# Performance work log

Measured on AMD Instinct MI355X. Metric: run time of the kernel, lower is better.

## Reference

```python
import jax, jax.numpy as jnp
import numpy as np

B, N, DEG, LOOKBACK, DIM, OUT = 256, 512, 16, 5, 64, 6
E = B * N * DEG            # 2,097,152 directed edges
NN = B * N                 # 131,072 nodes
K1 = int(np.ceil(0.8 * N))    # 410 nodes kept per graph after pool1
K2 = int(np.ceil(0.8 * K1))   # 328 nodes kept per graph after pool2


def setup_inputs():
    key = jax.random.key(0)
    ks = jax.random.split(key, 14)
    x = jax.random.normal(ks[0], (NN, LOOKBACK), jnp.float32)
    # per-graph random edges, then shift into the global node index space
    local = jax.random.randint(ks[1], (2, E), 0, N)
    offsets = jnp.repeat(jnp.arange(B, dtype=jnp.int32) * N, N * DEG)
    edge_index = local + offsets[None, :]

    def lin(k, fi, fo):
        return jax.random.normal(k, (fi, fo), jnp.float32) / np.sqrt(fi)

    return {
        "x": x,
        "edge_index": edge_index,
        "c1_Wl": lin(ks[2], LOOKBACK, DIM), "c1_bl": jnp.zeros((DIM,), jnp.float32),
        "c1_Wr": lin(ks[3], LOOKBACK, DIM),
        "pool1_w": jax.random.normal(ks[4], (DIM,), jnp.float32) / np.sqrt(DIM),
        "c2_Wl": lin(ks[5], DIM, DIM), "c2_bl": jnp.zeros((DIM,), jnp.float32),
        "c2_Wr": lin(ks[6], DIM, DIM),
        "pool2_w": jax.random.normal(ks[7], (DIM,), jnp.float32) / np.sqrt(DIM),
        "lin1_W": lin(ks[8], 2 * DIM, DIM), "lin1_b": jnp.zeros((DIM,), jnp.float32),
        "lin2_W": lin(ks[9], DIM, OUT), "lin2_b": jnp.zeros((OUT,), jnp.float32),
    }


def _sage(x, src, dst, valid, Wl, bl, Wr, n_nodes):
    # PyG SAGEConv: out = lin_l(mean_{j->i} x_j) + lin_r(x_i); empty nbhd -> 0
    msg = x[src] * valid[:, None]
    s = jax.ops.segment_sum(msg, dst, num_segments=n_nodes)
    deg = jax.ops.segment_sum(valid, dst, num_segments=n_nodes)
    mean = s / jnp.maximum(deg, 1.0)[:, None]
    return mean @ Wl + bl + x @ Wr


def _topk(x, w, nb, npg, k):
    # PyG TopKPooling: score = tanh(x.w/||w||), keep top-k per graph, scale kept rows
    score = jnp.tanh((x @ w) / jnp.linalg.norm(w))
    vals, idx = jax.lax.top_k(score.reshape(nb, npg), k)     # [nb, k]
    perm = (idx + (jnp.arange(nb) * npg)[:, None]).reshape(-1)
    return x[perm] * vals.reshape(-1, 1), perm


def _readout(x, nb, k):
    r = x.reshape(nb, k, -1)
    return jnp.concatenate([r.max(axis=1), r.mean(axis=1)], axis=1)  # [gmp | gap]


def reference(x, edge_index, c1_Wl, c1_bl, c1_Wr, pool1_w,
              c2_Wl, c2_bl, c2_Wr, pool2_w, lin1_W, lin1_b, lin2_W, lin2_b):
    src, dst = edge_index[0], edge_index[1]
    valid0 = jnp.ones((E,), jnp.float32)

    h = jax.nn.relu(_sage(x, src, dst, valid0, c1_Wl, c1_bl, c1_Wr, NN))
    h, perm1 = _topk(h, pool1_w, B, N, K1)
    x1 = _readout(h, B, K1)

    # filter_adj: remap edges to pooled node ids, mask dropped edges
    n1 = B * K1
    inv = jnp.full((NN,), -1, jnp.int32).at[perm1].set(jnp.arange(n1, dtype=jnp.int32))
    s1, d1 = inv[src], inv[dst]
    valid1 = ((s1 >= 0) & (d1 >= 0)).astype(jnp.float32)
    s1 = jnp.maximum(s1, 0)
    d1 = jnp.maximum(d1, 0)

    h = jax.nn.relu(_sage(h, s1, d1, valid1, c2_Wl, c2_bl, c2_Wr, n1))
    h, _ = _topk(h, pool2_w, B, K1, K2)
    x2 = _readout(h, B, K2)

    z = x1 + x2
    z = jax.nn.relu(z @ lin1_W + lin1_b)
    return z @ lin2_W + lin2_b
```

## Files before the change

kernel.cpp:

```cpp
#include <hip/hip_runtime.h>
#include <hip/hip_bf16.h>

#define BGR   256
#define NPG1  512
#define DEG   16
#define EPG   (NPG1 * DEG)
#define LB    5
#define DIM   64
#define OUTF  6
#define NN    (BGR * NPG1)
#define EDG   (BGR * EPG)
#define K1    410
#define K2    328
#define N1    (BGR * K1)
#define K1P   (K1 + 1)
#define NR    (BGR * K1P)
#define CSRW  48
#define CSRW1 56
#define RSTR  68
#define GRIDW (NR / 64)
#define GRIDA (N1 / 16)

__global__ __launch_bounds__(512)
void s1_csr_score_kernel(const float* __restrict__ x,
                         const int* __restrict__ eidx,
                         const float* __restrict__ Wl,
                         const float* __restrict__ bl,
                         const float* __restrict__ Wr,
                         const float* __restrict__ pw,
                         float* __restrict__ meanv,
                         float* __restrict__ sc1g) {
    __shared__ __align__(16) float xl[NPG1 * LB];
    __shared__ unsigned short lcsr[CSRW1 * NPG1];
    __shared__ int lcnt[NPG1];

    const int g = blockIdx.x, t = threadIdx.x;
    const int* __restrict__ src = eidx;
    const int* __restrict__ dst = eidx + EDG;

    {
        const float4* x4 = (const float4*)(x + (size_t)g * (NPG1 * LB));
        float4* xl4 = (float4*)xl;
        #pragma unroll
        for (int k = 0; k < 2; ++k) {
            int i = k * 512 + t;
            if (i < NPG1 * LB / 4) xl4[i] = x4[i];
        }
        lcnt[t] = 0;
    }
    __syncthreads();

    const int ebase = g * EPG;
    for (int k = 0; k < EPG / 512; ++k) {
        int e = ebase + k * 512 + t;
        int s = src[e] & (NPG1 - 1);
        int d = dst[e] & (NPG1 - 1);
        int slot = atomicAdd(&lcnt[d], 1);
        if (slot < CSRW1) lcsr[slot * NPG1 + d] = (unsigned short)s;
    }
    __syncthreads();

    const int dgf = lcnt[t];
    const int dg  = min(dgf, CSRW1);
    float s0 = 0.f, s1 = 0.f, s2 = 0.f, s3 = 0.f, s4 = 0.f;
    for (int k = 0; k < dg; ++k) {
        int s = lcsr[k * NPG1 + t];
        const float* xp = xl + s * LB;
        s0 += xp[0]; s1 += xp[1]; s2 += xp[2]; s3 += xp[3]; s4 += xp[4];
    }
    const float invd = 1.f / fmaxf((float)dgf, 1.f);
    float m[LB]  = { s0 * invd, s1 * invd, s2 * invd, s3 * invd, s4 * invd };
    float xv[LB];
    const int n = g * NPG1 + t;
    #pragma unroll
    for (int j = 0; j < LB; ++j) { xv[j] = xl[t * LB + j]; meanv[(size_t)n * LB + j] = m[j]; }

    const float4* Wl4 = (const float4*)Wl;
    const float4* Wr4 = (const float4*)Wr;
    const float4* bl4 = (const float4*)bl;
    const float4* pw4 = (const float4*)pw;
    float p = 0.f, q = 0.f;
    #pragma unroll 4
    for (int d4 = 0; d4 < DIM / 4; ++d4) {
        float4 bb = bl4[d4];
        float4 ww = pw4[d4];
        float4 h = bb;
        #pragma unroll
        for (int j = 0; j < LB; ++j) {
            float4 a = Wl4[j * (DIM / 4) + d4];
            float4 b = Wr4[j * (DIM / 4) + d4];
            h.x += m[j] * a.x + xv[j] * b.x;
            h.y += m[j] * a.y + xv[j] * b.y;
            h.z += m[j] * a.z + xv[j] * b.z;
            h.w += m[j] * a.w + xv[j] * b.w;
        }
        h.x = fmaxf(h.x, 0.f); h.y = fmaxf(h.y, 0.f);
        h.z = fmaxf(h.z, 0.f); h.w = fmaxf(h.w, 0.f);
        p += h.x * ww.x + h.y * ww.y + h.z * ww.z + h.w * ww.w;
        q += ww.x * ww.x + ww.y * ww.y + ww.z * ww.z + ww.w * ww.w;
    }
    sc1g[n] = tanhf(p / sqrtf(q));
}

__global__ __launch_bounds__(512)
void s1_rankpool_kernel(const float* __restrict__ x,
                        const float* __restrict__ meanv,
                        const float* __restrict__ sc1g,
                        const float* __restrict__ Wl,
                        const float* __restrict__ bl,
                        const float* __restrict__ Wr,
                        float* __restrict__ h1p,
                        int* __restrict__ invr,
                        float* __restrict__ x1buf) {
    __shared__ __align__(16) float sc[NPG1];
    __shared__ int   rnk[NPG1];
    __shared__ float redmx[8 * DIM];
    __shared__ float redsm[8 * DIM];

    const int g = blockIdx.x, t = threadIdx.x;
    const int wid = t >> 6, lane = t & 63;

    sc[t] = sc1g[g * NPG1 + t];
    if (t < DIM) h1p[((size_t)g * K1P + K1) * DIM + t] = 0.f;
    __syncthreads();

    {
        float my = sc[t];
        int r = 0;
        const float4* sc4 = (const float4*)sc;
        #pragma unroll 4
        for (int j4 = 0; j4 < NPG1 / 4; ++j4) {
            float4 v = sc4[j4];
            int j = 4 * j4;
            r += (v.x > my) | ((v.x == my) & (j     < t));
            r += (v.y > my) | ((v.y == my) & (j + 1 < t));
            r += (v.z > my) | ((v.z == my) & (j + 2 < t));
            r += (v.w > my) | ((v.w == my) & (j + 3 < t));
        }
        rnk[t] = r;
        invr[g * NPG1 + t] = (r < K1) ? r : -1;
    }
    __syncthreads();

    float wlv[LB], wrv[LB];
    #pragma unroll
    for (int j = 0; j < LB; ++j) { wlv[j] = Wl[j * DIM + lane]; wrv[j] = Wr[j * DIM + lane]; }
    const float blv = bl[lane];

    float mx = -INFINITY, sm = 0.f;
    for (int n = wid; n < NPG1; n += 8) {
        int r = rnk[n];
        if (r >= K1) continue;
        const float* mp = meanv + (size_t)(g * NPG1 + n) * LB;
        const float* xp = x + (size_t)(g * NPG1 + n) * LB;
        float al = 0.f, ar = 0.f;
        #pragma unroll
        for (int j = 0; j < LB; ++j) {
            al += mp[j] * wlv[j];
            ar += xp[j] * wrv[j];
        }
        float acc = fmaxf(blv + al + ar, 0.f);
        float v = acc * sc[n];
        h1p[((size_t)g * K1P + r) * DIM + lane] = v;
        mx = fmaxf(mx, v);
        sm += v;
    }
    redmx[wid * DIM + lane] = mx;
    redsm[wid * DIM + lane] = sm;
    __syncthreads();
    if (wid == 0) {
        float m2 = redmx[lane], s2 = redsm[lane];
        #pragma unroll
        for (int w = 1; w < 8; ++w) {
            m2 = fmaxf(m2, redmx[w * DIM + lane]);
            s2 += redsm[w * DIM + lane];
        }
        x1buf[g * 2 * DIM + lane]       = m2;
        x1buf[g * 2 * DIM + DIM + lane] = s2 * (1.0f / (float)K1);
    }
}

__global__ __launch_bounds__(512)
void csr2_build_kernel(const int* __restrict__ eidx,
                       const int* __restrict__ invr,
                       unsigned short* __restrict__ csr2,
                       int* __restrict__ indeg) {
    __shared__ short linv[NPG1];
    __shared__ __align__(16) unsigned short lcsr[K1 * CSRW];
    __shared__ int lcnt[K1];

    const int g = blockIdx.x, t = threadIdx.x;
    const int* __restrict__ src = eidx;
    const int* __restrict__ dst = eidx + EDG;

    if (t < NPG1) linv[t] = (short)invr[g * NPG1 + t];
    if (t < K1) lcnt[t] = 0;
    {
        const int fill = (K1 << 16) | K1;
        int* li = (int*)lcsr;
        for (int i = t; i < K1 * CSRW / 2; i += 512) li[i] = fill;
    }
    __syncthreads();

    const int ebase = g * EPG;
    for (int k = 0; k < EPG / 512; ++k) {
        int e = ebase + k * 512 + t;
        int rs = linv[src[e] & (NPG1 - 1)];
        int rd = linv[dst[e] & (NPG1 - 1)];
        if ((rs | rd) >= 0) {
            int slot = atomicAdd(&lcnt[rd], 1);
            if (slot < CSRW) lcsr[rd * CSRW + slot] = (unsigned short)rs;
        }
    }
    __syncthreads();

    {
        const int4* ls4 = (const int4*)lcsr;
        int4* gs4 = (int4*)(csr2 + (size_t)g * K1 * CSRW);
        for (int i = t; i < K1 * CSRW / 8; i += 512) gs4[i] = ls4[i];
        if (t < K1) indeg[g * K1 + t] = min(lcnt[t], CSRW);
    }
}

__global__ __launch_bounds__(256)
void gemm2_kernel(float* __restrict__ hY,
                  float* __restrict__ Yr,
                  const float* __restrict__ Wl,
                  const float* __restrict__ bl,
                  const float* __restrict__ Wr) {
    __shared__ __align__(16) float rt[64 * RSTR];

    const int t = threadIdx.x;
    const int nb = (int)blockIdx.x * 64;

    {
        const float4* G = (const float4*)&hY[(size_t)nb * DIM];
        #pragma unroll
        for (int k = 0; k < 4; ++k) {
            int c = k * 256 + t;
            int r = c >> 4, j4 = c & 15;
            *(float4*)&rt[r * RSTR + 4 * j4] = G[c];
        }
    }
    __syncthreads();

    const int lane = t & 63;
    const int wid  = __builtin_amdgcn_readfirstlane(t >> 6);
    const int cb   = (wid & 1) << 5;
    const bool isR = (wid & 2) != 0;
    const float* __restrict__ wmat = isR ? Wr : Wl;
    float* __restrict__ outp = isR ? Yr : hY;

    float rv[DIM];
    #pragma unroll
    for (int k = 0; k < DIM / 4; ++k) {
        float4 v = *(const float4*)&rt[lane * RSTR + 4 * k];
        rv[4 * k] = v.x; rv[4 * k + 1] = v.y; rv[4 * k + 2] = v.z; rv[4 * k + 3] = v.w;
    }

    float acc[32];
    #pragma unroll
    for (int c = 0; c < 32; ++c) acc[c] = 0.f;

    #pragma unroll
    for (int j = 0; j < DIM; ++j) {
        const float* __restrict__ wr_ = wmat + j * DIM + cb;
        #pragma unroll
        for (int c = 0; c < 32; ++c)
            acc[c] += rv[j] * wr_[c];
    }

    if (isR) {
        #pragma unroll
        for (int c = 0; c < 32; ++c) acc[c] += bl[cb + c];
    }

    float* orow = outp + (size_t)(nb + lane) * DIM + cb;
    #pragma unroll
    for (int k = 0; k < 8; ++k) {
        float4 v;
        v.x = acc[4 * k]; v.y = acc[4 * k + 1];
        v.z = acc[4 * k + 2]; v.w = acc[4 * k + 3];
        *(float4*)&orow[4 * k] = v;
    }
}

__global__ __launch_bounds__(256)
void gather2_kernel(const float* __restrict__ Yl,
                    float* __restrict__ Yh,
                    const unsigned short* __restrict__ csr2,
                    const int* __restrict__ indeg,
                    const float* __restrict__ pw,
                    float* __restrict__ sc2g) {
    const int t = threadIdx.x, wid = t >> 6, lane = t & 63;
    const int cid = ((int)blockIdx.x & 7) * (GRIDA / 8) + ((int)blockIdx.x >> 3);
    const int nb = __builtin_amdgcn_readfirstlane(cid * 16 + wid * 4);

    const float pwv = pw[lane];
    float q = pwv * pwv;
    #pragma unroll
    for (int o = 32; o; o >>= 1) q += __shfl_xor(q, o);
    const float inv_nrm = 1.f / sqrtf(q);

    #pragma unroll
    for (int i = 0; i < 4; ++i) {
        const int n  = nb + i;
        const int dg = indeg[n];
        const int g  = n / K1;
        const int lr = n - g * K1;
        const float* __restrict__ bp = Yl + (size_t)g * K1P * DIM;
        const int4* cr = (const int4*)(csr2 + (size_t)n * CSRW);
        float a0 = 0.f, a1 = 0.f;
        const int it = (dg + 7) >> 3;
        for (int kc = 0; kc < it; ++kc) {
            int4 wv = cr[kc];
            a0 += bp[((wv.x & 0xffff) << 6) + lane];
            a1 += bp[((wv.x >> 16)    << 6) + lane];
            a0 += bp[((wv.y & 0xffff) << 6) + lane];
            a1 += bp[((wv.y >> 16)    << 6) + lane];
            a0 += bp[((wv.z & 0xffff) << 6) + lane];
            a1 += bp[((wv.z >> 16)    << 6) + lane];
            a0 += bp[((wv.w & 0xffff) << 6) + lane];
            a1 += bp[((wv.w >> 16)    << 6) + lane];
        }
        const float invd = 1.f / fmaxf((float)dg, 1.f);
        float* yrow = Yh + (size_t)(g * K1P + lr) * DIM;
        const float h = fmaxf((a0 + a1) * invd + yrow[lane], 0.f);
        yrow[lane] = h;
        float p = h * pwv;
        #pragma unroll
        for (int o = 32; o; o >>= 1) p += __shfl_xor(p, o);
        if (lane == 0) sc2g[n] = tanhf(p * inv_nrm);
    }
}

__global__ __launch_bounds__(512)
void pool2_mlp_kernel(const float* __restrict__ sc2g,
                      const float* __restrict__ h2,
                      const float* __restrict__ x1buf,
                      const float* __restrict__ W1,
                      const float* __restrict__ b1,
                      const float* __restrict__ W2,
                      const float* __restrict__ b2,
                      float* __restrict__ out) {
    __shared__ __align__(16) float sc2[412];
    __shared__ int   rnk2[K1];
    __shared__ float redmx[8 * DIM];
    __shared__ float redsm[8 * DIM];
    __shared__ float zy[2 * DIM + DIM];

    const int g = blockIdx.x, t = threadIdx.x;
    const int wid = t >> 6, lane = t & 63;

    if (t < K1) sc2[t] = sc2g[g * K1 + t];
    if (t >= K1 && t < 412) sc2[t] = -INFINITY;
    __syncthreads();

    if (t < K1) {
        float my = sc2[t];
        int r = 0;
        const float4* sc4 = (const float4*)sc2;
        #pragma unroll 4
        for (int j4 = 0; j4 < 103; ++j4) {
            float4 v = sc4[j4];
            int j = 4 * j4;
            r += (v.x > my) | ((v.x == my) & (j     < t));
            r += (v.y > my) | ((v.y == my) & (j + 1 < t));
            r += (v.z > my) | ((v.z == my) & (j + 2 < t));
            r += (v.w > my) | ((v.w == my) & (j + 3 < t));
        }
        rnk2[t] = r;
    }
    __syncthreads();

    float mx = -INFINITY, sm = 0.f;
    for (int n = wid; n < K1; n += 8) {
        if (rnk2[n] < K2) {
            float v = h2[((size_t)g * K1P + n) * DIM + lane] * sc2[n];
            mx = fmaxf(mx, v);
            sm += v;
        }
    }
    redmx[wid * DIM + lane] = mx;
    redsm[wid * DIM + lane] = sm;
    __syncthreads();
    if (wid == 0) {
        float m2 = redmx[lane], s2 = redsm[lane];
        #pragma unroll
        for (int w = 1; w < 8; ++w) {
            m2 = fmaxf(m2, redmx[w * DIM + lane]);
            s2 += redsm[w * DIM + lane];
        }
        zy[lane]       = x1buf[g * 2 * DIM + lane]       + m2;
        zy[DIM + lane] = x1buf[g * 2 * DIM + DIM + lane] + s2 * (1.0f / (float)K2);
    }
    __syncthreads();

    if (t < DIM) {
        float a = b1[t];
        #pragma unroll 8
        for (int j = 0; j < 2 * DIM; ++j) a += zy[j] * W1[j * DIM + t];
        zy[2 * DIM + t] = fmaxf(a, 0.f);
    }
    __syncthreads();
    if (t < OUTF) {
        float a = b2[t];
        #pragma unroll
        for (int j = 0; j < DIM; ++j) a += zy[2 * DIM + j] * W2[j * OUTF + t];
        out[g * OUTF + t] = a;
    }
}

extern "C" void kernel_launch(void* const* d_in, const int* in_sizes, int n_in,
                              void* d_out, int out_size, void* d_ws, size_t ws_size,
                              hipStream_t stream) {
    (void)in_sizes; (void)n_in; (void)out_size; (void)ws_size;
    const float* x       = (const float*)d_in[0];
    const int*   eidx    = (const int*)d_in[1];
    const float* c1_Wl   = (const float*)d_in[2];
    const float* c1_bl   = (const float*)d_in[3];
    const float* c1_Wr   = (const float*)d_in[4];
    const float* pool1_w = (const float*)d_in[5];
    const float* c2_Wl   = (const float*)d_in[6];
    const float* c2_bl   = (const float*)d_in[7];
    const float* c2_Wr   = (const float*)d_in[8];
    const float* pool2_w = (const float*)d_in[9];
    const float* lin1_W  = (const float*)d_in[10];
    const float* lin1_b  = (const float*)d_in[11];
    const float* lin2_W  = (const float*)d_in[12];
    const float* lin2_b  = (const float*)d_in[13];
    float* out = (float*)d_out;

    char* w = (char*)d_ws;
    size_t off = 0;
    auto alloc = [&](size_t bytes) {
        void* p = w + off;
        off = (off + bytes + 255) & ~(size_t)255;
        return p;
    };
    float* h1p   = (float*)alloc((size_t)NR * DIM * 4);
    int*   invr  = (int*)  alloc((size_t)NN * 4);
    float* x1buf = (float*)alloc((size_t)BGR * 2 * DIM * 4);
    float* sc2g  = (float*)alloc((size_t)N1 * 4);
    int*   indeg = (int*)  alloc((size_t)N1 * 4);
    float* Yh    = (float*)alloc((size_t)NR * DIM * 4);
    char*  csreg = (char*) alloc((size_t)N1 * CSRW * 2);

    float* Yl    = h1p;
    unsigned short* csr2 = (unsigned short*)csreg;
    float* meanv = (float*)csreg;
    float* sc1g  = meanv + (size_t)NN * LB;

    s1_csr_score_kernel<<<BGR, 512, 0, stream>>>(x, eidx, c1_Wl, c1_bl, c1_Wr,
                                                 pool1_w, meanv, sc1g);
    s1_rankpool_kernel<<<BGR, 512, 0, stream>>>(x, meanv, sc1g, c1_Wl, c1_bl,
                                                c1_Wr, h1p, invr, x1buf);
    csr2_build_kernel<<<BGR, 512, 0, stream>>>(eidx, invr, csr2, indeg);
    gemm2_kernel<<<GRIDW, 256, 0, stream>>>(h1p, Yh, c2_Wl, c2_bl, c2_Wr);
    gather2_kernel<<<GRIDA, 256, 0, stream>>>(Yl, Yh, csr2, indeg, pool2_w, sc2g);
    pool2_mlp_kernel<<<BGR, 512, 0, stream>>>(sc2g, Yh, x1buf, lin1_W, lin1_b,
                                              lin2_W, lin2_b, out);
}
```

Measured before the change: 188.5 us.

## Register-tile layer-2 GEMM with transposed weights staged in LDS

A small prologue kernel transposes and concatenates the conv2 Wl and Wr matrices into one weight buffer. gemm2 now processes 128 rows per block and stages both the activation tile and the swizzled transposed weights in LDS. Each thread computes an 8x8 output micro-tile from float4 LDS reads, replacing per-lane row registers fed by uniform global weight loads. This aims to raise arithmetic intensity per LDS access and halve the block count. The costs are an extra kernel launch, more LDS per block, and float4 accesses at a 65-float row stride that are not 16-byte aligned.

New measurement: 184.3 us. -2.3%, faster.

```diff
diff --git a/kernel.cpp b/kernel.cpp
--- a/kernel.cpp
+++ b/kernel.cpp
@@ -17,8 +17,8 @@
 #define NR    (BGR * K1P)
 #define CSRW  48
 #define CSRW1 56
-#define RSTR  68
-#define GRIDW (NR / 64)
+#define RSTR  65
+#define GRIDW (NR / 128)
 #define GRIDA (N1 / 16)
 
 __global__ __launch_bounds__(512)
@@ -223,65 +223,87 @@
 }
 
 __global__ __launch_bounds__(256)
+void wtrans_kernel(const float* __restrict__ Wl,
+                   const float* __restrict__ Wr,
+                   float* __restrict__ WT) {
+    int i = blockIdx.x * 256 + threadIdx.x;
+    int c = i >> 6, j = i & 63;
+    WT[i] = (c < DIM) ? Wl[j * DIM + c] : Wr[j * DIM + (c - DIM)];
+}
+
+__global__ __launch_bounds__(256, 2)
 void gemm2_kernel(float* __restrict__ hY,
                   float* __restrict__ Yr,
-                  const float* __restrict__ Wl,
-                  const float* __restrict__ bl,
-                  const float* __restrict__ Wr) {
-    __shared__ __align__(16) float rt[64 * RSTR];
+                  const float* __restrict__ WT,
+                  const float* __restrict__ bl) {
+    __shared__ __align__(16) float rt[128 * RSTR];
+    __shared__ __align__(16) float wt[128 * DIM];
 
     const int t = threadIdx.x;
-    const int nb = (int)blockIdx.x * 64;
+    const int nb = (int)blockIdx.x * 128;
 
     {
         const float4* G = (const float4*)&hY[(size_t)nb * DIM];
         #pragma unroll
-        for (int k = 0; k < 4; ++k) {
-            int c = k * 256 + t;
-            int r = c >> 4, j4 = c & 15;
-            *(float4*)&rt[r * RSTR + 4 * j4] = G[c];
-        }
-    }
-    __syncthreads();
-
-    const int lane = t & 63;
-    const int wid  = __builtin_amdgcn_readfirstlane(t >> 6);
-    const int cb   = (wid & 1) << 5;
-    const bool isR = (wid & 2) != 0;
-    const float* __restrict__ wmat = isR ? Wr : Wl;
+        for (int k = 0; k < 8; ++k) {
+            int c4 = k * 256 + t;
+            int r = c4 >> 4, j4 = c4 & 15;
+            *(float4*)&rt[r * RSTR + 4 * j4] = G[c4];
+        }
+        const float4* WT4 = (const float4*)WT;
+        #pragma unroll
+        for (int k = 0; k < 8; ++k) {
+            int c4 = k * 256 + t;
+            int c = c4 >> 4, j4 = c4 & 15;
+            *(float4*)&wt[c * DIM + 4 * (j4 ^ ((c >> 3) & 7))] = WT4[c4];
+        }
+    }
+    __syncthreads();
+
+    const int tx = t & 15, ty = t >> 4;
+    const int r0 = ty * 8;
+    const int c0 = tx * 8;
+    const int sw = tx & 7;
+
+    float acc[8][8];
+    #pragma unroll
+    for (int i = 0; i < 8; ++i)
+        #pragma unroll
+        for (int k = 0; k < 8; ++k) acc[i][k] = 0.f;
+
+    #pragma unroll 2
+    for (int j4 = 0; j4 < 16; ++j4) {
+        float4 rv[8], wv[8];
+        #pragma unroll
+        for (int i = 0; i < 8; ++i)
+            rv[i] = *(const float4*)&rt[(r0 + i) * RSTR + 4 * j4];
+        #pragma unroll
+        for (int k = 0; k < 8; ++k)
+            wv[k] = *(const float4*)&wt[(c0 + k) * DIM + 4 * (j4 ^ sw)];
+        #pragma unroll
+        for (int i = 0; i < 8; ++i)
+            #pragma unroll
+            for (int k = 0; k < 8; ++k)
+                acc[i][k] += rv[i].x * wv[k].x + rv[i].y * wv[k].y
+                           + rv[i].z * wv[k].z + rv[i].w * wv[k].w;
+    }
+
+    const bool isR = tx >= 8;
+    const int cc = isR ? c0 - DIM : c0;
+    float bv[8];
+    #pragma unroll
+    for (int k = 0; k < 8; ++k) bv[k] = isR ? bl[cc + k] : 0.f;
     float* __restrict__ outp = isR ? Yr : hY;
-
-    float rv[DIM];
-    #pragma unroll
-    for (int k = 0; k < DIM / 4; ++k) {
-        float4 v = *(const float4*)&rt[lane * RSTR + 4 * k];
-        rv[4 * k] = v.x; rv[4 * k + 1] = v.y; rv[4 * k + 2] = v.z; rv[4 * k + 3] = v.w;
-    }
-
-    float acc[32];
-    #pragma unroll
-    for (int c = 0; c < 32; ++c) acc[c] = 0.f;
-
-    #pragma unroll
-    for (int j = 0; j < DIM; ++j) {
-        const float* __restrict__ wr_ = wmat + j * DIM + cb;
-        #pragma unroll
-        for (int c = 0; c < 32; ++c)
-            acc[c] += rv[j] * wr_[c];
-    }
-
-    if (isR) {
-        #pragma unroll
-        for (int c = 0; c < 32; ++c) acc[c] += bl[cb + c];
-    }
-
-    float* orow = outp + (size_t)(nb + lane) * DIM + cb;
-    #pragma unroll
-    for (int k = 0; k < 8; ++k) {
-        float4 v;
-        v.x = acc[4 * k]; v.y = acc[4 * k + 1];
-        v.z = acc[4 * k + 2]; v.w = acc[4 * k + 3];
-        *(float4*)&orow[4 * k] = v;
+    #pragma unroll
+    for (int i = 0; i < 8; ++i) {
+        float* orow = outp + (size_t)(nb + r0 + i) * DIM + cc;
+        float4 v0, v1;
+        v0.x = acc[i][0] + bv[0]; v0.y = acc[i][1] + bv[1];
+        v0.z = acc[i][2] + bv[2]; v0.w = acc[i][3] + bv[3];
+        v1.x = acc[i][4] + bv[4]; v1.y = acc[i][5] + bv[5];
+        v1.z = acc[i][6] + bv[6]; v1.w = acc[i][7] + bv[7];
+        *(float4*)&orow[0] = v0;
+        *(float4*)&orow[4] = v1;
     }
 }
 
@@ -443,6 +465,7 @@
     float* x1buf = (float*)alloc((size_t)BGR * 2 * DIM * 4);
     float* sc2g  = (float*)alloc((size_t)N1 * 4);
     int*   indeg = (int*)  alloc((size_t)N1 * 4);
+    float* WT    = (float*)alloc((size_t)128 * DIM * 4);
     float* Yh    = (float*)alloc((size_t)NR * DIM * 4);
     char*  csreg = (char*) alloc((size_t)N1 * CSRW * 2);
 
@@ -451,12 +474,13 @@
     float* meanv = (float*)csreg;
     float* sc1g  = meanv + (size_t)NN * LB;
 
+    wtrans_kernel<<<32, 256, 0, stream>>>(c2_Wl, c2_Wr, WT);
     s1_csr_score_kernel<<<BGR, 512, 0, stream>>>(x, eidx, c1_Wl, c1_bl, c1_Wr,
                                                  pool1_w, meanv, sc1g);
     s1_rankpool_kernel<<<BGR, 512, 0, stream>>>(x, meanv, sc1g, c1_Wl, c1_bl,
                                                 c1_Wr, h1p, invr, x1buf);
     csr2_build_kernel<<<BGR, 512, 0, stream>>>(eidx, invr, csr2, indeg);
-    gemm2_kernel<<<GRIDW, 256, 0, stream>>>(h1p, Yh, c2_Wl, c2_bl, c2_Wr);
+    gemm2_kernel<<<GRIDW, 256, 0, stream>>>(h1p, Yh, WT, c2_bl);
     gather2_kernel<<<GRIDA, 256, 0, stream>>>(Yl, Yh, csr2, indeg, pool2_w, sc2g);
     pool2_mlp_kernel<<<BGR, 512, 0, stream>>>(sc2g, Yh, x1buf, lin1_W, lin1_b,
                                               lin2_W, lin2_b, out);
```
